# Kernel optimization log

Measured on AMD Instinct MI355X. Metric: run time of the kernel, lower is better.

Reference implementation:

```python
import jax, jax.numpy as jnp
import numpy as np

D = 1024      # d_model
H = 16        # num_heads
DH = D // H   # head_dim = 64
BASE = 10000.0


def setup_inputs() -> dict:
    key = jax.random.key(0)
    ks = jax.random.split(key, 5)
    lengths = np.array([1024, 768, 896, 1024], dtype=np.int32)
    cu = np.concatenate([[0], np.cumsum(lengths)]).astype(np.int32)
    T = int(cu[-1])  # 3712 packed tokens
    x = jax.random.normal(ks[0], (T, D), dtype=jnp.float32)
    Wqkv = jax.random.normal(ks[1], (D, 3 * D), dtype=jnp.float32) / np.sqrt(D)
    bqkv = jax.random.normal(ks[2], (3 * D,), dtype=jnp.float32) * 0.02
    Wo = jax.random.normal(ks[3], (D, D), dtype=jnp.float32) / np.sqrt(D)
    bo = jax.random.normal(ks[4], (D,), dtype=jnp.float32) * 0.02
    return {"x": x, "Wqkv": Wqkv, "bqkv": bqkv, "Wo": Wo, "bo": bo,
            "cu_seqlens": jnp.asarray(cu), "max_seqlen": 1024}


def reference(x, Wqkv, bqkv, Wo, bo, cu_seqlens, max_seqlen):
    T = x.shape[0]
    B = cu_seqlens.shape[0] - 1
    S = int(max_seqlen)

    # fused qkv projection: [T, 3, H, DH]
    qkv = (x @ Wqkv + bqkv).reshape(T, 3, H, DH)
    q, k, v = qkv[:, 0], qkv[:, 1], qkv[:, 2]

    # per-token sequence id and within-sequence position (RoPE resets per seq)
    tok = jnp.arange(T)
    seq_id = jnp.searchsorted(cu_seqlens, tok, side='right') - 1  # [T]
    pos = tok - cu_seqlens[seq_id]                                # [T]

    # RoPE, non-interleaved (rotate-half over full head_dim)
    inv_freq = 1.0 / (BASE ** (jnp.arange(0, DH, 2, dtype=jnp.float32) / DH))
    ang = pos[:, None].astype(jnp.float32) * inv_freq             # [T, DH/2]
    cos = jnp.cos(ang)[:, None, :]                                # [T, 1, DH/2]
    sin = jnp.sin(ang)[:, None, :]

    def rope(t):
        t1, t2 = t[..., : DH // 2], t[..., DH // 2:]
        return jnp.concatenate([t1 * cos - t2 * sin, t2 * cos + t1 * sin], axis=-1)

    q, k = rope(q), rope(k)

    # scatter packed tokens into padded [B, S, H, DH] (varlen attention)
    qp = jnp.zeros((B, S, H, DH), x.dtype).at[seq_id, pos].set(q)
    kp = jnp.zeros((B, S, H, DH), x.dtype).at[seq_id, pos].set(k)
    vp = jnp.zeros((B, S, H, DH), x.dtype).at[seq_id, pos].set(v)
    valid = jnp.zeros((B, S), bool).at[seq_id, pos].set(True)

    scale = 1.0 / np.sqrt(DH)
    scores = jnp.einsum('bqhd,bkhd->bhqk', qp, kp) * scale        # [B,H,S,S]
    causal = jnp.tril(jnp.ones((S, S), bool))
    mask = causal[None, None] & valid[:, None, None, :]
    scores = jnp.where(mask, scores, jnp.asarray(-1e30, scores.dtype))
    attn = jax.nn.softmax(scores, axis=-1)
    op = jnp.einsum('bhqk,bkhd->bqhd', attn, vp)                  # [B,S,H,DH]

    # unpad back to packed layout, then output projection (W_o)
    out = op[seq_id, pos].reshape(T, D)
    return out @ Wo + bo
```

## Files before the change

kernel.cpp:

```cpp
#include <hip/hip_runtime.h>

typedef _Float16 f16;
typedef _Float16 f16x8 __attribute__((ext_vector_type(8)));
typedef _Float16 f16x4 __attribute__((ext_vector_type(4)));
typedef float f32x4 __attribute__((ext_vector_type(4)));

#define MFMA16(a, b, c) __builtin_amdgcn_mfma_f32_16x16x32_f16((a), (b), (c), 0, 0, 0)

typedef __attribute__((address_space(3))) void lds_void;
typedef const __attribute__((address_space(1))) void g_void;
__device__ __forceinline__ void async_copy16(void* lds, const void* g) {
    __builtin_amdgcn_global_load_lds((g_void*)g, (lds_void*)lds, 16, 0, 0);
}

__global__ void cvt_x(const float* __restrict__ in, f16* __restrict__ out, int n) {
    int i4 = (blockIdx.x * 256 + threadIdx.x) * 4;
    if (i4 >= n) return;
    float4 v = *reinterpret_cast<const float4*>(in + i4);
    f16x4 o;
    o[0] = (f16)v.x; o[1] = (f16)v.y; o[2] = (f16)v.z; o[3] = (f16)v.w;
    *reinterpret_cast<f16x4*>(out + i4) = o;
}

__global__ void trig_tab(float2* __restrict__ tab, int Spad) {
    int idx = blockIdx.x * 256 + threadIdx.x;
    if (idx >= Spad * 32) return;
    int pos = idx >> 5, i = idx & 31;
    float inv = exp2f((float)i * (-13.287712379549449f / 32.f));
    float sn, cs;
    __sincosf((float)pos * inv, &sn, &cs);
    tab[idx] = make_float2(cs, sn);
}

__global__ void wtrans2(const float* __restrict__ Wqkv, const float* __restrict__ Wo,
                        f16* __restrict__ outQkv, f16* __restrict__ outWo) {
    __shared__ f16 tile[64][65];
    int id = blockIdx.x;
    const float* in; f16* out; int N, bx, by;
    if (id < 768) { in = Wqkv; out = outQkv; N = 3072; bx = id % 48; by = id / 48; }
    else { id -= 768; in = Wo; out = outWo; N = 1024; bx = id % 16; by = id / 16; }
    const int K = 1024;
    int n0 = bx * 64, k0 = by * 64;
    int c = threadIdx.x & 63, rb = threadIdx.x >> 6;
#pragma unroll
    for (int it = 0; it < 16; ++it) {
        int r = rb + it * 4;
        tile[r][c] = (f16)in[(size_t)(k0 + r) * N + n0 + c];
    }
    __syncthreads();
#pragma unroll
    for (int it = 0; it < 16; ++it) {
        int rr = rb + it * 4;
        out[(size_t)(n0 + rr) * K + k0 + c] = tile[c][rr];
    }
}

#define BM 128
#define BN 128
#define BKK 32
__global__ __launch_bounds__(256) void gemm_tile(
    const f16* __restrict__ A, const f16* __restrict__ Bt,
    const float* __restrict__ bias, f16* __restrict__ Ch, float* __restrict__ Cf,
    int M, int N, int K, int nbx) {
    __shared__ f16 lA[2][BM * BKK];
    __shared__ f16 lB[2][BN * BKK];
    int tid = threadIdx.x;
    int lane = tid & 63, w = tid >> 6;
    int lr = lane & 15, lg = lane >> 4;
    int wm = (w & 1) * 64, wn = (w >> 1) * 64;

    int nwg = gridDim.x, wg = blockIdx.x;
    int tile = ((nwg & 7) == 0) ? ((wg & 7) * (nwg >> 3) + (wg >> 3)) : wg;
    int by = tile / nbx, bx = tile % nbx;

    int srow = tid >> 2;
    int scol = (tid & 3) * 8;
    const f16* ga0 = A  + (size_t)min(by * BM + srow,      M - 1) * K + scol;
    const f16* ga1 = A  + (size_t)min(by * BM + 64 + srow, M - 1) * K + scol;
    const f16* gb0 = Bt + (size_t)min(bx * BN + srow,      N - 1) * K + scol;
    const f16* gb1 = Bt + (size_t)min(bx * BN + 64 + srow, N - 1) * K + scol;

    f32x4 acc[4][4] = {};
    int NT = K / BKK;

#define STAGE(curb, kt) do {                                        \
        int ko = (kt) * BKK;                                        \
        async_copy16(&lA[curb][w * 512],        ga0 + ko);          \
        async_copy16(&lA[curb][2048 + w * 512], ga1 + ko);          \
        async_copy16(&lB[curb][w * 512],        gb0 + ko);          \
        async_copy16(&lB[curb][2048 + w * 512], gb1 + ko);          \
    } while (0)

    STAGE(0, 0);
    __syncthreads();
    int cur = 0;
    for (int kt = 0; kt < NT; ++kt) {
        if (kt + 1 < NT) STAGE(cur ^ 1, kt + 1);
        f16x8 af[4], bf[4];
#pragma unroll
        for (int i = 0; i < 4; ++i) {
            af[i] = *reinterpret_cast<const f16x8*>(&lA[cur][(wm + i * 16 + lr) * BKK + lg * 8]);
            bf[i] = *reinterpret_cast<const f16x8*>(&lB[cur][(wn + i * 16 + lr) * BKK + lg * 8]);
        }
#pragma unroll
        for (int mi = 0; mi < 4; ++mi)
#pragma unroll
            for (int ni = 0; ni < 4; ++ni)
                acc[mi][ni] = MFMA16(af[mi], bf[ni], acc[mi][ni]);
        __syncthreads();
        cur ^= 1;
    }
#undef STAGE

#pragma unroll
    for (int mi = 0; mi < 4; ++mi) {
#pragma unroll
        for (int ni = 0; ni < 4; ++ni) {
            int col = bx * BN + wn + ni * 16 + lr;
            float bv = bias ? bias[col] : 0.f;
#pragma unroll
            for (int r = 0; r < 4; ++r) {
                int row = by * BM + wm + mi * 16 + 4 * lg + r;
                if (row >= M) continue;
                float v = acc[mi][ni][r] + bv;
                if (Ch) Ch[(size_t)row * N + col] = (f16)v;
                else    Cf[(size_t)row * N + col] = v;
            }
        }
    }
}

__global__ __launch_bounds__(256) void rope_v(
    const f16* __restrict__ qkv, const int* __restrict__ cu,
    const float2* __restrict__ tab, int Bn, int T, int Spad,
    f16* __restrict__ qh2, f16* __restrict__ kh2, f16* __restrict__ vt) {
    __shared__ f16 tile[64][65];
    int h = blockIdx.y;
    int t0 = blockIdx.x * 64;
    int tid = threadIdx.x;
    int c = tid & 63, rb = tid >> 6;
#pragma unroll
    for (int it = 0; it < 16; ++it) {
        int r = rb + it * 4;
        int t = t0 + r;
        f16 v = (f16)0.f;
        if (t < T) v = qkv[(size_t)t * 3072 + 2048 + h * 64 + c];
        tile[r][c] = v;
    }
    int tok = t0 + (tid >> 2);
    int g = tid & 3;
    if (tok < T) {
        int b = 0, pos = tok;
        for (int q = 0; q < Bn; ++q) {
            int lo = cu[q], hi = cu[q + 1];
            if (tok >= lo && tok < hi) { b = q; pos = tok - lo; break; }
        }
        const f16* qp = qkv + (size_t)tok * 3072 + h * 64 + g * 8;
        f16x8 q1 = *reinterpret_cast<const f16x8*>(qp);
        f16x8 q2 = *reinterpret_cast<const f16x8*>(qp + 32);
        f16x8 k1 = *reinterpret_cast<const f16x8*>(qp + 1024);
        f16x8 k2 = *reinterpret_cast<const f16x8*>(qp + 1056);
        const float2* tb = tab + pos * 32 + g * 8;
        f16x8 qo1, qo2, ko1, ko2;
#pragma unroll
        for (int e = 0; e < 8; ++e) {
            float2 csn = tb[e];
            float cs = csn.x, sn = csn.y;
            float a = (float)q1[e], bq = (float)q2[e];
            float ka = (float)k1[e], kb = (float)k2[e];
            qo1[e] = (f16)((a * cs - bq * sn) * 0.125f);
            qo2[e] = (f16)((bq * cs + a * sn) * 0.125f);
            ko1[e] = (f16)(ka * cs - kb * sn);
            ko2[e] = (f16)(kb * cs + ka * sn);
        }
        size_t ob = ((size_t)(b * 16 + h) * Spad + pos) * 64 + g * 8;
        *reinterpret_cast<f16x8*>(qh2 + ob)      = qo1;
        *reinterpret_cast<f16x8*>(qh2 + ob + 32) = qo2;
        *reinterpret_cast<f16x8*>(kh2 + ob)      = ko1;
        *reinterpret_cast<f16x8*>(kh2 + ob + 32) = ko2;
    }
    __syncthreads();
    int t = t0 + c;
    int bb = 0, pos2 = -1;
    if (t < T) {
        for (int q = 0; q < Bn; ++q) {
            int lo = cu[q], hi = cu[q + 1];
            if (t >= lo && t < hi) { bb = q; pos2 = t - lo; }
        }
    }
#pragma unroll
    for (int it = 0; it < 16; ++it) {
        int d = rb + it * 4;
        if (pos2 >= 0) vt[((size_t)(bb * 16 + h) * 64 + d) * Spad + pos2] = tile[c][d];
    }
}

__global__ __launch_bounds__(128) void attn_fwd(
    const f16* __restrict__ qh2, const f16* __restrict__ kh2,
    const f16* __restrict__ vt, const int* __restrict__ cu,
    f16* __restrict__ oh, int Spad, int nq, int Bn) {
    int wgid = blockIdx.x;
    int nbh = Bn * 16;
    int b, h, qi;
    if ((nbh & 7) == 0) {
        int xcd = wgid & 7, rest = wgid >> 3, nbh8 = nbh >> 3;
        int bhhi = rest % nbh8;
        qi = (nq - 1) - rest / nbh8;
        int bhv = (bhhi << 3) | xcd;
        b = bhv >> 4; h = bhv & 15;
    } else {
        qi = wgid % nq;
        int bhv = wgid / nq;
        b = bhv >> 4; h = bhv & 15;
    }
    int bh = b * 16 + h;
    int s0 = cu[b];
    int len = cu[b + 1] - s0;
    int q0 = qi * 32;
    if (q0 >= len) return;
    int tid = threadIdx.x;
    int wv = tid >> 6;
    int lane = tid & 63, lr = lane & 15, lg = lane >> 4;
    __shared__ f16 pl[2][2][16][40];
    __shared__ float mlb[2][2][16];
    __shared__ f32x4 owb[2][4][16][4];

    const f16* qbase = qh2 + (size_t)bh * Spad * 64;
    const f16* kbase = kh2 + (size_t)bh * Spad * 64;
    const f16* vbase = vt  + (size_t)bh * 64 * Spad;

    f16x8 qf[2][2];
#pragma unroll
    for (int qt = 0; qt < 2; ++qt) {
        const f16* qp = qbase + (size_t)(q0 + 16 * qt + lr) * 64 + 8 * lg;
        qf[qt][0] = *reinterpret_cast<const f16x8*>(qp);
        qf[qt][1] = *reinterpret_cast<const f16x8*>(qp + 32);
    }
    float mrun[2] = {-1e30f, -1e30f}, lrun[2] = {0.f, 0.f};
    f32x4 oacc[2][4] = {};

    int kend = min(q0 + 32, len);
    int ntk = (kend + 31) >> 5;

    f16x8 kf[2][2], kn[2][2];
#pragma unroll
    for (int j = 0; j < 2; ++j) {
        const f16* kp = kbase + (size_t)(wv * 32 + 16 * j + lr) * 64 + 8 * lg;
        kf[j][0] = *reinterpret_cast<const f16x8*>(kp);
        kf[j][1] = *reinterpret_cast<const f16x8*>(kp + 32);
    }

    for (int kt = wv; kt < ntk; kt += 2) {
        int kk0 = kt << 5;
        f16x8 vf[4];
#pragma unroll
        for (int dt = 0; dt < 4; ++dt)
            vf[dt] = *reinterpret_cast<const f16x8*>(
                vbase + (size_t)(16 * dt + lr) * Spad + kk0 + 8 * lg);
        f32x4 st[2][2];
#pragma unroll
        for (int qt = 0; qt < 2; ++qt)
#pragma unroll
            for (int j = 0; j < 2; ++j) {
                f32x4 z = {0, 0, 0, 0};
                z = MFMA16(kf[j][0], qf[qt][0], z);
                z = MFMA16(kf[j][1], qf[qt][1], z);
                st[qt][j] = z;
            }
        if (kt + 2 < ntk) {
#pragma unroll
            for (int j = 0; j < 2; ++j) {
                const f16* kp = kbase + (size_t)(kk0 + 64 + 16 * j + lr) * 64 + 8 * lg;
                kn[j][0] = *reinterpret_cast<const f16x8*>(kp);
                kn[j][1] = *reinterpret_cast<const f16x8*>(kp + 32);
            }
        }
#pragma unroll
        for (int qt = 0; qt < 2; ++qt) {
            int qr = q0 + 16 * qt + lr;
            float sv[2][4];
            float mx = -1e30f;
#pragma unroll
            for (int j = 0; j < 2; ++j)
#pragma unroll
                for (int r = 0; r < 4; ++r) {
                    int kc = kk0 + 16 * j + 4 * lg + r;
                    float v = st[qt][j][r];
                    if (kc > qr || kc >= len) v = -1e30f;
                    sv[j][r] = v;
                    mx = fmaxf(mx, v);
                }
            mx = fmaxf(mx, __shfl_xor(mx, 16, 64));
            mx = fmaxf(mx, __shfl_xor(mx, 32, 64));
            float mnew = fmaxf(mrun[qt], mx);
            float al = __expf(mrun[qt] - mnew);
            mrun[qt] = mnew;
            float rs = 0.f;
            f16x4 pk0, pk1;
#pragma unroll
            for (int r = 0; r < 4; ++r) {
                float p0 = __expf(sv[0][r] - mnew);
                float p1 = __expf(sv[1][r] - mnew);
                rs += p0 + p1;
                pk0[r] = (f16)p0;
                pk1[r] = (f16)p1;
            }
            rs += __shfl_xor(rs, 16, 64);
            rs += __shfl_xor(rs, 32, 64);
            lrun[qt] = lrun[qt] * al + rs;
            *reinterpret_cast<f16x4*>(&pl[wv][qt][lr][4 * lg])      = pk0;
            *reinterpret_cast<f16x4*>(&pl[wv][qt][lr][16 + 4 * lg]) = pk1;
#pragma unroll
            for (int dt = 0; dt < 4; ++dt)
#pragma unroll
                for (int r = 0; r < 4; ++r) oacc[qt][dt][r] *= al;
        }
        asm volatile("s_waitcnt lgkmcnt(0)" ::: "memory");
        __builtin_amdgcn_sched_barrier(0);
        f16x8 pa0 = *reinterpret_cast<const f16x8*>(&pl[wv][0][lr][8 * lg]);
        f16x8 pa1 = *reinterpret_cast<const f16x8*>(&pl[wv][1][lr][8 * lg]);
#pragma unroll
        for (int dt = 0; dt < 4; ++dt) {
            oacc[0][dt] = MFMA16(vf[dt], pa0, oacc[0][dt]);
            oacc[1][dt] = MFMA16(vf[dt], pa1, oacc[1][dt]);
        }
        asm volatile("" ::: "memory");
#pragma unroll
        for (int j = 0; j < 2; ++j) {
            kf[j][0] = kn[j][0];
            kf[j][1] = kn[j][1];
        }
    }

    if (wv == 1) {
#pragma unroll
        for (int qt = 0; qt < 2; ++qt) {
            if (lg == 0) { mlb[qt][0][lr] = mrun[qt]; mlb[qt][1][lr] = lrun[qt]; }
#pragma unroll
            for (int dt = 0; dt < 4; ++dt)
                owb[qt][dt][lr][lg] = oacc[qt][dt];
        }
    }
    __syncthreads();
    if (wv == 0) {
#pragma unroll
        for (int qt = 0; qt < 2; ++qt) {
            int qr = q0 + 16 * qt + lr;
            if (qr >= len) continue;
            float m1 = mlb[qt][0][lr], l1 = mlb[qt][1][lr];
            float mnew = fmaxf(mrun[qt], m1);
            float a0 = __expf(mrun[qt] - mnew);
            float a1 = __expf(m1 - mnew);
            float linv = 1.f / (lrun[qt] * a0 + l1 * a1);
            f16* orow = oh + (size_t)(s0 + qr) * 1024 + h * 64;
#pragma unroll
            for (int dt = 0; dt < 4; ++dt) {
                f32x4 o1 = owb[qt][dt][lr][lg];
                f16x4 ov;
#pragma unroll
                for (int r = 0; r < 4; ++r)
                    ov[r] = (f16)((oacc[qt][dt][r] * a0 + o1[r] * a1) * linv);
                *reinterpret_cast<f16x4*>(orow + 16 * dt + 4 * lg) = ov;
            }
        }
    }
}

extern "C" void kernel_launch(void* const* d_in, const int* in_sizes, int n_in,
                              void* d_out, int out_size, void* d_ws, size_t ws_size,
                              hipStream_t stream) {
    const float* x    = (const float*)d_in[0];
    const float* Wqkv = (const float*)d_in[1];
    const float* bqkv = (const float*)d_in[2];
    const float* Wo   = (const float*)d_in[3];
    const float* bo   = (const float*)d_in[4];
    const int*   cu   = (const int*)d_in[5];

    const int Dm = 1024;
    int T  = in_sizes[0] / Dm;
    int Bn = in_sizes[5] - 1;
    int Spad = 1024;

    auto al = [](size_t v) { return (v + 255) & ~(size_t)255; };
    char* w = (char*)d_ws;
    size_t off = 0;
    f16* xh     = (f16*)(w + off); off = al(off + (size_t)2 * T * 1024);
    f16* qkvh   = (f16*)(w + off); off = al(off + (size_t)2 * T * 3072);
    f16* wqkvT  = (f16*)(w + off); off = al(off + (size_t)2 * 3072 * 1024);
    f16* woT    = (f16*)(w + off); off = al(off + (size_t)2 * 1024 * 1024);
    f16* qh2    = (f16*)(w + off); off = al(off + (size_t)2 * Bn * 16 * 64 * (size_t)Spad);
    f16* kh2    = (f16*)(w + off); off = al(off + (size_t)2 * Bn * 16 * 64 * (size_t)Spad);
    f16* vtp    = (f16*)(w + off); off = al(off + (size_t)2 * Bn * 16 * 64 * (size_t)Spad);
    f16* ohp    = (f16*)(w + off); off = al(off + (size_t)2 * T * 1024);
    float2* tab = (float2*)(w + off); off = al(off + (size_t)8 * Spad * 32);
    (void)ws_size;

    {
        int n = T * 1024;
        cvt_x<<<(n / 4 + 255) / 256, 256, 0, stream>>>(x, xh, n);
    }
    trig_tab<<<(Spad * 32 + 255) / 256, 256, 0, stream>>>(tab, Spad);
    wtrans2<<<768 + 256, 256, 0, stream>>>(Wqkv, Wo, wqkvT, woT);
    {
        int nbx = 3072 / BN, nby = (T + BM - 1) / BM;
        gemm_tile<<<nbx * nby, 256, 0, stream>>>(xh, wqkvT, bqkv, qkvh, nullptr, T, 3072, 1024, nbx);
    }
    rope_v<<<dim3((T + 63) / 64, 16), 256, 0, stream>>>(qkvh, cu, tab, Bn, T, Spad, qh2, kh2, vtp);
    {
        int nq = Spad / 32;
        int ngrid = nq * 16 * Bn;
        attn_fwd<<<ngrid, 128, 0, stream>>>(qh2, kh2, vtp, cu, ohp, Spad, nq, Bn);
    }
    {
        int nbx = 1024 / BN, nby = (T + BM - 1) / BM;
        gemm_tile<<<nbx * nby, 256, 0, stream>>>(ohp, woT, bo, nullptr, (float*)d_out, T, 1024, 1024, nbx);
    }
}
```

Before: 132.6 us.

## Fuse RoPE and V transpose into QKV GEMM epilogue, merge prep kernels

Moves the RoPE rotation, Q scaling and the V transposed scatter into the epilogue of the QKV projection GEMM, so the intermediate packed qkv buffer and the separate rope_v kernel go away. Because the head-dim pairs (d, d+32) sit in the same lane's accumulators, the rotation can be done in registers. The input cast, trig-table build and weight transposes are merged into one prep launch to cut launch overhead. In exchange, the epilogue now does a per-row sequence search and scalar, less coalesced stores into the Q/K layout, which may slow the GEMM tail.

```diff
diff --git a/kernel.cpp b/kernel.cpp
--- a/kernel.cpp
+++ b/kernel.cpp
@@ -5,6 +5,10 @@
 typedef _Float16 f16x4 __attribute__((ext_vector_type(4)));
 typedef float f32x4 __attribute__((ext_vector_type(4)));
 
+#define BM 128
+#define BN 128
+#define BKK 32
+
 #define MFMA16(a, b, c) __builtin_amdgcn_mfma_f32_16x16x32_f16((a), (b), (c), 0, 0, 0)
 
 typedef __attribute__((address_space(3))) void lds_void;
@@ -13,76 +17,66 @@
     __builtin_amdgcn_global_load_lds((g_void*)g, (lds_void*)lds, 16, 0, 0);
 }
 
-__global__ void cvt_x(const float* __restrict__ in, f16* __restrict__ out, int n) {
-    int i4 = (blockIdx.x * 256 + threadIdx.x) * 4;
-    if (i4 >= n) return;
-    float4 v = *reinterpret_cast<const float4*>(in + i4);
-    f16x4 o;
-    o[0] = (f16)v.x; o[1] = (f16)v.y; o[2] = (f16)v.z; o[3] = (f16)v.w;
-    *reinterpret_cast<f16x4*>(out + i4) = o;
-}
-
-__global__ void trig_tab(float2* __restrict__ tab, int Spad) {
-    int idx = blockIdx.x * 256 + threadIdx.x;
-    if (idx >= Spad * 32) return;
-    int pos = idx >> 5, i = idx & 31;
-    float inv = exp2f((float)i * (-13.287712379549449f / 32.f));
-    float sn, cs;
-    __sincosf((float)pos * inv, &sn, &cs);
-    tab[idx] = make_float2(cs, sn);
-}
-
-__global__ void wtrans2(const float* __restrict__ Wqkv, const float* __restrict__ Wo,
-                        f16* __restrict__ outQkv, f16* __restrict__ outWo) {
-    __shared__ f16 tile[64][65];
+__global__ __launch_bounds__(256) void prep(
+    const float* __restrict__ x, f16* __restrict__ xh, int T,
+    const float* __restrict__ Wqkv, const float* __restrict__ Wo,
+    f16* __restrict__ wqkvT, f16* __restrict__ woT,
+    float2* __restrict__ tab, int Spad) {
     int id = blockIdx.x;
-    const float* in; f16* out; int N, bx, by;
-    if (id < 768) { in = Wqkv; out = outQkv; N = 3072; bx = id % 48; by = id / 48; }
-    else { id -= 768; in = Wo; out = outWo; N = 1024; bx = id % 16; by = id / 16; }
-    const int K = 1024;
-    int n0 = bx * 64, k0 = by * 64;
-    int c = threadIdx.x & 63, rb = threadIdx.x >> 6;
-#pragma unroll
-    for (int it = 0; it < 16; ++it) {
-        int r = rb + it * 4;
-        tile[r][c] = (f16)in[(size_t)(k0 + r) * N + n0 + c];
-    }
-    __syncthreads();
-#pragma unroll
-    for (int it = 0; it < 16; ++it) {
-        int rr = rb + it * 4;
-        out[(size_t)(n0 + rr) * K + k0 + c] = tile[c][rr];
-    }
-}
-
-#define BM 128
-#define BN 128
-#define BKK 32
-__global__ __launch_bounds__(256) void gemm_tile(
+    int tid = threadIdx.x;
+    if (id < 1024) {
+        __shared__ f16 tile[64][65];
+        const float* in; f16* out; int N, bx, by;
+        if (id < 768) { in = Wqkv; out = wqkvT; N = 3072; bx = id % 48; by = id / 48; }
+        else { int j = id - 768; in = Wo; out = woT; N = 1024; bx = j % 16; by = j / 16; }
+        const int K = 1024;
+        int n0 = bx * 64, k0 = by * 64;
+        int c = tid & 63, rb = tid >> 6;
+#pragma unroll
+        for (int it = 0; it < 16; ++it) {
+            int r = rb + it * 4;
+            tile[r][c] = (f16)in[(size_t)(k0 + r) * N + n0 + c];
+        }
+        __syncthreads();
+#pragma unroll
+        for (int it = 0; it < 16; ++it) {
+            int rr = rb + it * 4;
+            out[(size_t)(n0 + rr) * K + k0 + c] = tile[c][rr];
+        }
+    } else if (id < 1152) {
+        int idx = (id - 1024) * 256 + tid;
+        if (idx < Spad * 32) {
+            int pos = idx >> 5, i = idx & 31;
+            float inv = exp2f((float)i * (-13.287712379549449f / 32.f));
+            float sn, cs;
+            __sincosf((float)pos * inv, &sn, &cs);
+            tab[idx] = make_float2(cs, sn);
+        }
+    } else {
+        int i4 = ((id - 1152) * 256 + tid) * 4;
+        if (i4 < T * 1024) {
+            float4 v = *reinterpret_cast<const float4*>(x + i4);
+            f16x4 o;
+            o[0] = (f16)v.x; o[1] = (f16)v.y; o[2] = (f16)v.z; o[3] = (f16)v.w;
+            *reinterpret_cast<f16x4*>(xh + i4) = o;
+        }
+    }
+}
+
+__device__ __forceinline__ void gemm_core(
     const f16* __restrict__ A, const f16* __restrict__ Bt,
-    const float* __restrict__ bias, f16* __restrict__ Ch, float* __restrict__ Cf,
-    int M, int N, int K, int nbx) {
-    __shared__ f16 lA[2][BM * BKK];
-    __shared__ f16 lB[2][BN * BKK];
-    int tid = threadIdx.x;
+    int M, int N, int K, int bx, int by, int tid,
+    f16 lA[2][BM * BKK], f16 lB[2][BN * BKK], f32x4 acc[4][4]) {
     int lane = tid & 63, w = tid >> 6;
     int lr = lane & 15, lg = lane >> 4;
     int wm = (w & 1) * 64, wn = (w >> 1) * 64;
-
-    int nwg = gridDim.x, wg = blockIdx.x;
-    int tile = ((nwg & 7) == 0) ? ((wg & 7) * (nwg >> 3) + (wg >> 3)) : wg;
-    int by = tile / nbx, bx = tile % nbx;
-
     int srow = tid >> 2;
     int scol = (tid & 3) * 8;
     const f16* ga0 = A  + (size_t)min(by * BM + srow,      M - 1) * K + scol;
     const f16* ga1 = A  + (size_t)min(by * BM + 64 + srow, M - 1) * K + scol;
     const f16* gb0 = Bt + (size_t)min(bx * BN + srow,      N - 1) * K + scol;
     const f16* gb1 = Bt + (size_t)min(bx * BN + 64 + srow, N - 1) * K + scol;
-
-    f32x4 acc[4][4] = {};
     int NT = K / BKK;
-
 #define STAGE(curb, kt) do {                                        \
         int ko = (kt) * BKK;                                        \
         async_copy16(&lA[curb][w * 512],        ga0 + ko);          \
@@ -90,7 +84,6 @@
         async_copy16(&lB[curb][w * 512],        gb0 + ko);          \
         async_copy16(&lB[curb][2048 + w * 512], gb1 + ko);          \
     } while (0)
-
     STAGE(0, 0);
     __syncthreads();
     int cur = 0;
@@ -111,87 +104,126 @@
         cur ^= 1;
     }
 #undef STAGE
-
+}
+
+__global__ __launch_bounds__(256) void gemm_qkv(
+    const f16* __restrict__ A, const f16* __restrict__ Bt,
+    const float* __restrict__ bias, const int* __restrict__ cu,
+    const float2* __restrict__ tab, int M, int Bn, int Spad,
+    f16* __restrict__ qh2, f16* __restrict__ kh2, f16* __restrict__ vt, int nbx) {
+    __shared__ f16 lA[2][BM * BKK];
+    __shared__ f16 lB[2][BN * BKK];
+    int tid = threadIdx.x;
+    int nwg = gridDim.x, wg = blockIdx.x;
+    int tile = ((nwg & 7) == 0) ? ((wg & 7) * (nwg >> 3) + (wg >> 3)) : wg;
+    int by = tile / nbx, bx = tile % nbx;
+
+    f32x4 acc[4][4] = {};
+    gemm_core(A, Bt, M, 3072, 1024, bx, by, tid, lA, lB, acc);
+
+    int lane = tid & 63, w = tid >> 6;
+    int lr = lane & 15, lg = lane >> 4;
+    int wm = (w & 1) * 64, wn = (w >> 1) * 64;
+    int colwave = bx * BN + wn;
+    int sect = colwave >> 10;
+    int h = (colwave & 1023) >> 6;
+    float bv[4];
+#pragma unroll
+    for (int ni = 0; ni < 4; ++ni) bv[ni] = bias[colwave + ni * 16 + lr];
+
+#pragma unroll
+    for (int mi = 0; mi < 4; ++mi) {
+        int row0 = by * BM + wm + mi * 16 + 4 * lg;
+        if (row0 >= M) continue;
+        if (sect == 2) {
+            int b0 = 0, p0 = row0;
+            for (int q = 0; q < Bn; ++q) {
+                int lo = cu[q], hi = cu[q + 1];
+                if (row0 >= lo && row0 < hi) { b0 = q; p0 = row0 - lo; break; }
+            }
+            bool pack = (row0 + 3 < M) && ((p0 & 3) == 0) && (row0 + 3 < cu[b0 + 1]);
+            if (pack) {
+                size_t vb = (size_t)(b0 * 16 + h) * 64;
+#pragma unroll
+                for (int ni = 0; ni < 4; ++ni) {
+                    int d = ni * 16 + lr;
+                    f16x4 ov;
+#pragma unroll
+                    for (int r = 0; r < 4; ++r) ov[r] = (f16)(acc[mi][ni][r] + bv[ni]);
+                    *reinterpret_cast<f16x4*>(vt + (vb + d) * Spad + p0) = ov;
+                }
+            } else {
+                for (int r = 0; r < 4; ++r) {
+                    int row = row0 + r;
+                    if (row >= M) break;
+                    int b = 0, pos = row;
+                    for (int q = 0; q < Bn; ++q) {
+                        int lo = cu[q], hi = cu[q + 1];
+                        if (row >= lo && row < hi) { b = q; pos = row - lo; break; }
+                    }
+                    size_t vb = (size_t)(b * 16 + h) * 64;
+#pragma unroll
+                    for (int ni = 0; ni < 4; ++ni)
+                        vt[(vb + ni * 16 + lr) * Spad + pos] = (f16)(acc[mi][ni][r] + bv[ni]);
+                }
+            }
+        } else {
+            float sc = sect == 0 ? 0.125f : 1.f;
+            f16* dstbase = sect == 0 ? qh2 : kh2;
+            for (int r = 0; r < 4; ++r) {
+                int row = row0 + r;
+                if (row >= M) break;
+                int b = 0, pos = row;
+                for (int q = 0; q < Bn; ++q) {
+                    int lo = cu[q], hi = cu[q + 1];
+                    if (row >= lo && row < hi) { b = q; pos = row - lo; break; }
+                }
+                const float2* tb = tab + pos * 32;
+                f16* dst = dstbase + ((size_t)(b * 16 + h) * Spad + pos) * 64;
+#pragma unroll
+                for (int p = 0; p < 2; ++p) {
+                    int i = p * 16 + lr;
+                    float2 csn = tb[i];
+                    float v1 = acc[mi][p][r] + bv[p];
+                    float v2 = acc[mi][p + 2][r] + bv[p + 2];
+                    dst[i]      = (f16)((v1 * csn.x - v2 * csn.y) * sc);
+                    dst[i + 32] = (f16)((v2 * csn.x + v1 * csn.y) * sc);
+                }
+            }
+        }
+    }
+}
+
+__global__ __launch_bounds__(256) void gemm_out(
+    const f16* __restrict__ A, const f16* __restrict__ Bt,
+    const float* __restrict__ bias, float* __restrict__ Cf,
+    int M, int N, int K, int nbx) {
+    __shared__ f16 lA[2][BM * BKK];
+    __shared__ f16 lB[2][BN * BKK];
+    int tid = threadIdx.x;
+    int nwg = gridDim.x, wg = blockIdx.x;
+    int tile = ((nwg & 7) == 0) ? ((wg & 7) * (nwg >> 3) + (wg >> 3)) : wg;
+    int by = tile / nbx, bx = tile % nbx;
+
+    f32x4 acc[4][4] = {};
+    gemm_core(A, Bt, M, N, K, bx, by, tid, lA, lB, acc);
+
+    int lane = tid & 63, w = tid >> 6;
+    int lr = lane & 15, lg = lane >> 4;
+    int wm = (w & 1) * 64, wn = (w >> 1) * 64;
 #pragma unroll
     for (int mi = 0; mi < 4; ++mi) {
 #pragma unroll
         for (int ni = 0; ni < 4; ++ni) {
             int col = bx * BN + wn + ni * 16 + lr;
-            float bv = bias ? bias[col] : 0.f;
+            float bvv = bias[col];
 #pragma unroll
             for (int r = 0; r < 4; ++r) {
                 int row = by * BM + wm + mi * 16 + 4 * lg + r;
                 if (row >= M) continue;
-                float v = acc[mi][ni][r] + bv;
-                if (Ch) Ch[(size_t)row * N + col] = (f16)v;
-                else    Cf[(size_t)row * N + col] = v;
-            }
-        }
-    }
-}
-
-__global__ __launch_bounds__(256) void rope_v(
-    const f16* __restrict__ qkv, const int* __restrict__ cu,
-    const float2* __restrict__ tab, int Bn, int T, int Spad,
-    f16* __restrict__ qh2, f16* __restrict__ kh2, f16* __restrict__ vt) {
-    __shared__ f16 tile[64][65];
-    int h = blockIdx.y;
-    int t0 = blockIdx.x * 64;
-    int tid = threadIdx.x;
-    int c = tid & 63, rb = tid >> 6;
-#pragma unroll
-    for (int it = 0; it < 16; ++it) {
-        int r = rb + it * 4;
-        int t = t0 + r;
-        f16 v = (f16)0.f;
-        if (t < T) v = qkv[(size_t)t * 3072 + 2048 + h * 64 + c];
-        tile[r][c] = v;
-    }
-    int tok = t0 + (tid >> 2);
-    int g = tid & 3;
-    if (tok < T) {
-        int b = 0, pos = tok;
-        for (int q = 0; q < Bn; ++q) {
-            int lo = cu[q], hi = cu[q + 1];
-            if (tok >= lo && tok < hi) { b = q; pos = tok - lo; break; }
-        }
-        const f16* qp = qkv + (size_t)tok * 3072 + h * 64 + g * 8;
-        f16x8 q1 = *reinterpret_cast<const f16x8*>(qp);
-        f16x8 q2 = *reinterpret_cast<const f16x8*>(qp + 32);
-        f16x8 k1 = *reinterpret_cast<const f16x8*>(qp + 1024);
-        f16x8 k2 = *reinterpret_cast<const f16x8*>(qp + 1056);
-        const float2* tb = tab + pos * 32 + g * 8;
-        f16x8 qo1, qo2, ko1, ko2;
-#pragma unroll
-        for (int e = 0; e < 8; ++e) {
-            float2 csn = tb[e];
-            float cs = csn.x, sn = csn.y;
-            float a = (float)q1[e], bq = (float)q2[e];
-            float ka = (float)k1[e], kb = (float)k2[e];
-            qo1[e] = (f16)((a * cs - bq * sn) * 0.125f);
-            qo2[e] = (f16)((bq * cs + a * sn) * 0.125f);
-            ko1[e] = (f16)(ka * cs - kb * sn);
-            ko2[e] = (f16)(kb * cs + ka * sn);
-        }
-        size_t ob = ((size_t)(b * 16 + h) * Spad + pos) * 64 + g * 8;
-        *reinterpret_cast<f16x8*>(qh2 + ob)      = qo1;
-        *reinterpret_cast<f16x8*>(qh2 + ob + 32) = qo2;
-        *reinterpret_cast<f16x8*>(kh2 + ob)      = ko1;
-        *reinterpret_cast<f16x8*>(kh2 + ob + 32) = ko2;
-    }
-    __syncthreads();
-    int t = t0 + c;
-    int bb = 0, pos2 = -1;
-    if (t < T) {
-        for (int q = 0; q < Bn; ++q) {
-            int lo = cu[q], hi = cu[q + 1];
-            if (t >= lo && t < hi) { bb = q; pos2 = t - lo; }
-        }
-    }
-#pragma unroll
-    for (int it = 0; it < 16; ++it) {
-        int d = rb + it * 4;
-        if (pos2 >= 0) vt[((size_t)(bb * 16 + h) * 64 + d) * Spad + pos2] = tile[c][d];
+                Cf[(size_t)row * N + col] = acc[mi][ni][r] + bvv;
+            }
+        }
     }
 }
 
@@ -385,7 +417,6 @@
     char* w = (char*)d_ws;
     size_t off = 0;
     f16* xh     = (f16*)(w + off); off = al(off + (size_t)2 * T * 1024);
-    f16* qkvh   = (f16*)(w + off); off = al(off + (size_t)2 * T * 3072);
     f16* wqkvT  = (f16*)(w + off); off = al(off + (size_t)2 * 3072 * 1024);
     f16* woT    = (f16*)(w + off); off = al(off + (size_t)2 * 1024 * 1024);
     f16* qh2    = (f16*)(w + off); off = al(off + (size_t)2 * Bn * 16 * 64 * (size_t)Spad);
@@ -395,17 +426,12 @@
     float2* tab = (float2*)(w + off); off = al(off + (size_t)8 * Spad * 32);
     (void)ws_size;
 
-    {
-        int n = T * 1024;
-        cvt_x<<<(n / 4 + 255) / 256, 256, 0, stream>>>(x, xh, n);
-    }
-    trig_tab<<<(Spad * 32 + 255) / 256, 256, 0, stream>>>(tab, Spad);
-    wtrans2<<<768 + 256, 256, 0, stream>>>(Wqkv, Wo, wqkvT, woT);
+    prep<<<1152 + T, 256, 0, stream>>>(x, xh, T, Wqkv, Wo, wqkvT, woT, tab, Spad);
     {
         int nbx = 3072 / BN, nby = (T + BM - 1) / BM;
-        gemm_tile<<<nbx * nby, 256, 0, stream>>>(xh, wqkvT, bqkv, qkvh, nullptr, T, 3072, 1024, nbx);
-    }
-    rope_v<<<dim3((T + 63) / 64, 16), 256, 0, stream>>>(qkvh, cu, tab, Bn, T, Spad, qh2, kh2, vtp);
+        gemm_qkv<<<nbx * nby, 256, 0, stream>>>(xh, wqkvT, bqkv, cu, tab,
+                                                T, Bn, Spad, qh2, kh2, vtp, nbx);
+    }
     {
         int nq = Spad / 32;
         int ngrid = nq * 16 * Bn;
@@ -413,6 +439,7 @@
     }
     {
         int nbx = 1024 / BN, nby = (T + BM - 1) / BM;
-        gemm_tile<<<nbx * nby, 256, 0, stream>>>(ohp, woT, bo, nullptr, (float*)d_out, T, 1024, 1024, nbx);
-    }
-}
+        gemm_out<<<nbx * nby, 256, 0, stream>>>(ohp, woT, bo, (float*)d_out,
+                                                T, 1024, 1024, nbx);
+    }
+}
```

Measured after the change: 125.3 us. 1.06x faster.
